# Performance work log

Hardware: AMD Instinct MI355X
Metric: run time of the kernel (lower is better)

The kernel has to match this reference:

```python
import jax, jax.numpy as jnp
import numpy as np

N_NODES = 50000
N_EDGES = 800000
D_FEAT = 128
UNITS = 128


def setup_inputs() -> dict:
    key = jax.random.key(0)
    k1, k2, k3, k4, k5 = jax.random.split(key, 5)
    node_states = jax.random.normal(k1, (N_NODES, D_FEAT), dtype=jnp.float32)
    src = jnp.sort(jax.random.randint(k2, (N_EDGES,), 0, N_NODES))
    dst = jax.random.randint(k3, (N_EDGES,), 0, N_NODES)
    edges = jnp.stack([src, dst], axis=1).astype(jnp.int64)  # [E,2], sorted by source
    kernel = jax.random.normal(k4, (D_FEAT, UNITS), dtype=jnp.float32) * (1.0 / np.sqrt(D_FEAT))
    kernel_attention = jax.random.normal(k5, (2 * UNITS, 1), dtype=jnp.float32) * (1.0 / np.sqrt(2 * UNITS))
    return {"node_states": node_states, "edges": edges, "kernel": kernel, "kernel_attention": kernel_attention}


def reference(node_states, edges, kernel, kernel_attention):
    n_nodes = node_states.shape[0]
    src, dst = edges[:, 0], edges[:, 1]
    # linear transform of node features
    h = node_states @ kernel                                  # [N, U]
    # per-edge concatenated (src, dst) features -> raw attention logit
    e_feat = jnp.concatenate([h[src], h[dst]], axis=-1)       # [E, 2U]
    logits = jax.nn.leaky_relu((e_feat @ kernel_attention)[:, 0], negative_slope=0.2)  # [E]
    scores = jnp.exp(jnp.clip(logits, -2.0, 2.0))             # [E]
    # segment softmax over incoming edges of each source node
    denom = jax.ops.segment_sum(scores, src, num_segments=n_nodes)  # [N]
    alpha = scores / denom[src]                                # [E]
    # weighted aggregation of neighbor features
    out = jax.ops.segment_sum(h[dst] * alpha[:, None], src, num_segments=n_nodes)  # [N, U]
    return out
```

## Files before the change

### kernel.cpp

```cpp
#include <hip/hip_runtime.h>

#define N_NODES 50000
#define N_EDGES 800000
#define D 128
#define LDA 136

typedef __attribute__((ext_vector_type(8))) short bf16x8;
typedef __attribute__((ext_vector_type(4))) float f32x4;

__device__ __forceinline__ unsigned short f2bf(float f) {
    union { float f; unsigned u; } v; v.f = f;
    return (unsigned short)((v.u + 0x7fffu + ((v.u >> 16) & 1u)) >> 16);
}
__device__ __forceinline__ float bflo(unsigned u) {
    union { unsigned u; float f; } c; c.u = u << 16; return c.f;
}
__device__ __forceinline__ float bfhi(unsigned u) {
    union { unsigned u; float f; } c; c.u = u & 0xffff0000u; return c.f;
}

#define NB_SEARCH 196
__global__ void k1_prep(const int* __restrict__ edges, const float* __restrict__ W,
                        const float* __restrict__ ka, int* __restrict__ row_ptr,
                        unsigned short* __restrict__ Wt,
                        float* __restrict__ u, float* __restrict__ v) {
    int b = blockIdx.x, tid = threadIdx.x;
    if (b < NB_SEARCH) {
        int n = b * 256 + tid;
        if (n > N_NODES) return;
        int lo = 0, hi = N_EDGES;
        while (lo < hi) {
            int mid = (lo + hi) >> 1;
            if (edges[2 * mid] < n) lo = mid + 1; else hi = mid;
        }
        row_ptr[n] = lo;
    } else if (b < NB_SEARCH + 8) {
        int bi = b - NB_SEARCH;
        for (int i = tid; i < 16 * D; i += 256) {
            int n = bi * 16 + (i >> 7), k = i & 127;
            Wt[n * D + k] = f2bf(W[k * D + n]);
        }
    } else {
        int k = tid & 127;
        const float* kap = ka + ((tid >> 7) ? D : 0);
        float s = 0.f;
        for (int j = 0; j < D; ++j) s += W[k * D + j] * kap[j];
        if (tid < 128) u[k] = s; else v[k] = s;
    }
}

__global__ __launch_bounds__(256) void kh(const float* __restrict__ X,
                                          const unsigned short* __restrict__ Wt,
                                          const float* __restrict__ u,
                                          const float* __restrict__ v,
                                          unsigned short* __restrict__ h,
                                          float* __restrict__ a_src,
                                          float* __restrict__ a_dst) {
    __shared__ unsigned short As[128 * LDA];
    __shared__ unsigned short Bs[128 * LDA];
    int tid = threadIdx.x;
    int row0 = blockIdx.x * 128;

    for (int i = tid; i < 2048; i += 256) {
        int r = i >> 4, c = i & 15;
        *(uint4*)&Bs[r * LDA + c * 8] = *(const uint4*)&Wt[r * D + c * 8];
    }
    for (int i = tid; i < 2048; i += 256) {
        int r = i >> 4, c = i & 15;
        int gr = row0 + r;
        union { unsigned short us[8]; uint4 q; } pk;
        if (gr < N_NODES) {
            const float* xp = X + (size_t)gr * D + c * 8;
#pragma unroll
            for (int j = 0; j < 8; ++j) pk.us[j] = f2bf(xp[j]);
        } else pk.q = make_uint4(0u, 0u, 0u, 0u);
        *(uint4*)&As[r * LDA + c * 8] = pk.q;
    }
    __syncthreads();

    int wave = tid >> 6, lane = tid & 63;
    int m16 = lane & 15, quad = lane >> 4;
    int wr0 = wave * 32;
    f32x4 acc[2][8];
#pragma unroll
    for (int i = 0; i < 2; ++i)
#pragma unroll
        for (int j = 0; j < 8; ++j) acc[i][j] = (f32x4){0.f, 0.f, 0.f, 0.f};

    for (int k0 = 0; k0 < D; k0 += 32) {
        bf16x8 a0 = *(const bf16x8*)&As[(wr0 + m16) * LDA + k0 + quad * 8];
        bf16x8 a1 = *(const bf16x8*)&As[(wr0 + 16 + m16) * LDA + k0 + quad * 8];
#pragma unroll
        for (int j = 0; j < 8; ++j) {
            bf16x8 bf = *(const bf16x8*)&Bs[(j * 16 + m16) * LDA + k0 + quad * 8];
            acc[0][j] = __builtin_amdgcn_mfma_f32_16x16x32_bf16(a0, bf, acc[0][j], 0, 0, 0);
            acc[1][j] = __builtin_amdgcn_mfma_f32_16x16x32_bf16(a1, bf, acc[1][j], 0, 0, 0);
        }
    }

#pragma unroll
    for (int i = 0; i < 2; ++i)
#pragma unroll
        for (int j = 0; j < 8; ++j)
#pragma unroll
            for (int r = 0; r < 4; ++r) {
                int row = row0 + wr0 + i * 16 + quad * 4 + r;
                if (row < N_NODES)
                    h[(size_t)row * D + j * 16 + m16] = f2bf(acc[i][j][r]);
            }

    int rr = tid >> 1, hf = tid & 1;
    int grow = row0 + rr;
    if (grow < N_NODES) {
        const float* xp = X + (size_t)grow * D + hf * 64;
        float ps = 0.f, pd = 0.f;
        for (int jj = 0; jj < 64; jj += 4) {
            float4 xv = *(const float4*)(xp + jj);
            float4 uv = *(const float4*)(u + hf * 64 + jj);
            float4 vv = *(const float4*)(v + hf * 64 + jj);
            ps += xv.x * uv.x + xv.y * uv.y + xv.z * uv.z + xv.w * uv.w;
            pd += xv.x * vv.x + xv.y * vv.y + xv.z * vv.z + xv.w * vv.w;
        }
        ps += __shfl_xor(ps, 1, 64);
        pd += __shfl_xor(pd, 1, 64);
        if (hf == 0) { a_src[grow] = ps; a_dst[grow] = pd; }
    }
}

__global__ __launch_bounds__(256) void k3(const int* __restrict__ edges,
                                          const int* __restrict__ row_ptr,
                                          const unsigned short* __restrict__ h,
                                          const float* __restrict__ a_src,
                                          const float* __restrict__ a_dst,
                                          float* __restrict__ out) {
    int node = blockIdx.x * 4 + (threadIdx.x >> 6);
    if (node >= N_NODES) return;
    int lane = threadIdx.x & 63;
    int q = lane >> 4;
    int l16 = lane & 15;

    int start = row_ptr[node], end = row_ptr[node + 1];
    float asn = a_src[node];

    float4 accA = make_float4(0.f, 0.f, 0.f, 0.f);
    float4 accB = make_float4(0.f, 0.f, 0.f, 0.f);
    float dn = 0.f;

    for (int base = start; base < end; base += 64) {
        int cnt = min(64, end - base);
        int d = 0; float s = 0.f;
        if (lane < cnt) {
            d = edges[2 * (base + lane) + 1];
            float lg = asn + a_dst[d];
            lg = (lg >= 0.f) ? lg : 0.2f * lg;
            lg = fminf(fmaxf(lg, -2.f), 2.f);
            s = __expf(lg);
        }
        for (int j = 0; j < cnt; j += 8) {
            float s0 = __shfl(s, j + q, 64);
            int   d0 = __shfl(d, j + q, 64);
            float s1 = __shfl(s, j + q + 4, 64);
            int   d1 = __shfl(d, j + q + 4, 64);
            uint4 p0 = *(const uint4*)(h + ((size_t)d0 << 7) + (l16 << 3));
            uint4 p1 = *(const uint4*)(h + ((size_t)d1 << 7) + (l16 << 3));
            accA.x += s0 * bflo(p0.x); accA.y += s0 * bfhi(p0.x);
            accA.z += s0 * bflo(p0.y); accA.w += s0 * bfhi(p0.y);
            accB.x += s0 * bflo(p0.z); accB.y += s0 * bfhi(p0.z);
            accB.z += s0 * bflo(p0.w); accB.w += s0 * bfhi(p0.w);
            accA.x += s1 * bflo(p1.x); accA.y += s1 * bfhi(p1.x);
            accA.z += s1 * bflo(p1.y); accA.w += s1 * bfhi(p1.y);
            accB.x += s1 * bflo(p1.z); accB.y += s1 * bfhi(p1.z);
            accB.z += s1 * bflo(p1.w); accB.w += s1 * bfhi(p1.w);
            dn += s0 + s1;
        }
    }

    float vals[9] = {accA.x, accA.y, accA.z, accA.w,
                     accB.x, accB.y, accB.z, accB.w, dn};
#pragma unroll
    for (int m = 32; m >= 16; m >>= 1)
#pragma unroll
        for (int i = 0; i < 9; ++i) vals[i] += __shfl_xor(vals[i], m, 64);

    if (q == 0) {
        float inv = (end > start) ? 1.f / vals[8] : 0.f;
        float4 o0 = make_float4(vals[0] * inv, vals[1] * inv, vals[2] * inv, vals[3] * inv);
        float4 o1 = make_float4(vals[4] * inv, vals[5] * inv, vals[6] * inv, vals[7] * inv);
        float* op = out + (size_t)node * D + l16 * 8;
        *(float4*)op = o0;
        *(float4*)(op + 4) = o1;
    }
}

extern "C" void kernel_launch(void* const* d_in, const int* in_sizes, int n_in,
                              void* d_out, int out_size, void* d_ws, size_t ws_size,
                              hipStream_t stream) {
    const float* X     = (const float*)d_in[0];
    const int*   edges = (const int*)d_in[1];
    const float* W     = (const float*)d_in[2];
    const float* ka    = (const float*)d_in[3];

    char* ws = (char*)d_ws;
    unsigned short* h  = (unsigned short*)ws;
    float* a_src   = (float*)(ws + (size_t)N_NODES * D * 2);
    float* a_dst   = a_src + N_NODES;
    int*   row_ptr = (int*)(a_dst + N_NODES);
    unsigned short* Wt = (unsigned short*)(row_ptr + N_NODES + 4);
    float* u = (float*)(Wt + D * D);
    float* v = u + D;
    float* out = (float*)d_out;

    k1_prep<<<NB_SEARCH + 9, 256, 0, stream>>>(edges, W, ka, row_ptr, Wt, u, v);
    kh<<<(N_NODES + 127) / 128, 256, 0, stream>>>(X, Wt, u, v, h, a_src, a_dst);
    k3<<<(N_NODES + 3) / 4, 256, 0, stream>>>(edges, row_ptr, h, a_src, a_dst, out);
}
```

Baseline: 134.3 us.

## Fuse prep into GEMM kernel, derive attention logits from accumulators, widen gather

Merges the row-pointer search, weight transpose and projection into the GEMM kernel, so one launch handles both and every block converts W into shared memory itself. The per-node attention terms now come from the MFMA accumulators dotted with the attention vector, replacing a second read of X against precomputed u/v. The aggregation loop now issues four row gathers per iteration instead of two to get more loads in flight. The cost is redundant W conversion in every GEMM block, strided 2-byte LDS writes during that conversion, and attention logits computed from the bf16-rounded GEMM result instead of full-precision X.

```diff
diff --git a/kernel.cpp b/kernel.cpp
--- a/kernel.cpp
+++ b/kernel.cpp
@@ -5,6 +5,9 @@
 #define D 128
 #define LDA 136
 
+#define SEARCH_BLOCKS 196
+#define GEMM_BLOCKS   391
+
 typedef __attribute__((ext_vector_type(8))) short bf16x8;
 typedef __attribute__((ext_vector_type(4))) float f32x4;
 
@@ -19,13 +22,20 @@
     union { unsigned u; float f; } c; c.u = u & 0xffff0000u; return c.f;
 }
 
-#define NB_SEARCH 196
-__global__ void k1_prep(const int* __restrict__ edges, const float* __restrict__ W,
-                        const float* __restrict__ ka, int* __restrict__ row_ptr,
-                        unsigned short* __restrict__ Wt,
-                        float* __restrict__ u, float* __restrict__ v) {
+__global__ __launch_bounds__(256) void kh_fused(const float* __restrict__ X,
+                                                const int* __restrict__ edges,
+                                                const float* __restrict__ W,
+                                                const float* __restrict__ ka,
+                                                unsigned short* __restrict__ h,
+                                                float* __restrict__ a_src,
+                                                float* __restrict__ a_dst,
+                                                int* __restrict__ row_ptr) {
+    __shared__ unsigned short As[128 * LDA];
+    __shared__ unsigned short Bs[128 * LDA];
+    __shared__ float kas[2 * D];
     int b = blockIdx.x, tid = threadIdx.x;
-    if (b < NB_SEARCH) {
+
+    if (b < SEARCH_BLOCKS) {
         int n = b * 256 + tid;
         if (n > N_NODES) return;
         int lo = 0, hi = N_EDGES;
@@ -34,36 +44,18 @@
             if (edges[2 * mid] < n) lo = mid + 1; else hi = mid;
         }
         row_ptr[n] = lo;
-    } else if (b < NB_SEARCH + 8) {
-        int bi = b - NB_SEARCH;
-        for (int i = tid; i < 16 * D; i += 256) {
-            int n = bi * 16 + (i >> 7), k = i & 127;
-            Wt[n * D + k] = f2bf(W[k * D + n]);
-        }
-    } else {
-        int k = tid & 127;
-        const float* kap = ka + ((tid >> 7) ? D : 0);
-        float s = 0.f;
-        for (int j = 0; j < D; ++j) s += W[k * D + j] * kap[j];
-        if (tid < 128) u[k] = s; else v[k] = s;
-    }
-}
-
-__global__ __launch_bounds__(256) void kh(const float* __restrict__ X,
-                                          const unsigned short* __restrict__ Wt,
-                                          const float* __restrict__ u,
-                                          const float* __restrict__ v,
-                                          unsigned short* __restrict__ h,
-                                          float* __restrict__ a_src,
-                                          float* __restrict__ a_dst) {
-    __shared__ unsigned short As[128 * LDA];
-    __shared__ unsigned short Bs[128 * LDA];
-    int tid = threadIdx.x;
-    int row0 = blockIdx.x * 128;
-
-    for (int i = tid; i < 2048; i += 256) {
-        int r = i >> 4, c = i & 15;
-        *(uint4*)&Bs[r * LDA + c * 8] = *(const uint4*)&Wt[r * D + c * 8];
+        return;
+    }
+
+    int row0 = (b - SEARCH_BLOCKS) * 128;
+    kas[tid] = ka[tid];
+    for (int i = tid; i < 128 * 32; i += 256) {
+        int k = i >> 5, n4 = (i & 31) * 4;
+        float4 w = *(const float4*)(W + k * D + n4);
+        Bs[(n4 + 0) * LDA + k] = f2bf(w.x);
+        Bs[(n4 + 1) * LDA + k] = f2bf(w.y);
+        Bs[(n4 + 2) * LDA + k] = f2bf(w.z);
+        Bs[(n4 + 3) * LDA + k] = f2bf(w.w);
     }
     for (int i = tid; i < 2048; i += 256) {
         int r = i >> 4, c = i & 15;
@@ -109,22 +101,24 @@
                     h[(size_t)row * D + j * 16 + m16] = f2bf(acc[i][j][r]);
             }
 
-    int rr = tid >> 1, hf = tid & 1;
-    int grow = row0 + rr;
-    if (grow < N_NODES) {
-        const float* xp = X + (size_t)grow * D + hf * 64;
-        float ps = 0.f, pd = 0.f;
-        for (int jj = 0; jj < 64; jj += 4) {
-            float4 xv = *(const float4*)(xp + jj);
-            float4 uv = *(const float4*)(u + hf * 64 + jj);
-            float4 vv = *(const float4*)(v + hf * 64 + jj);
-            ps += xv.x * uv.x + xv.y * uv.y + xv.z * uv.z + xv.w * uv.w;
-            pd += xv.x * vv.x + xv.y * vv.y + xv.z * vv.z + xv.w * vv.w;
-        }
-        ps += __shfl_xor(ps, 1, 64);
-        pd += __shfl_xor(pd, 1, 64);
-        if (hf == 0) { a_src[grow] = ps; a_dst[grow] = pd; }
-    }
+#pragma unroll
+    for (int i = 0; i < 2; ++i)
+#pragma unroll
+        for (int r = 0; r < 4; ++r) {
+            float ps = 0.f, pd = 0.f;
+#pragma unroll
+            for (int j = 0; j < 8; ++j) {
+                float val = acc[i][j][r];
+                ps += val * kas[j * 16 + m16];
+                pd += val * kas[D + j * 16 + m16];
+            }
+            for (int off = 8; off > 0; off >>= 1) {
+                ps += __shfl_down(ps, off, 16);
+                pd += __shfl_down(pd, off, 16);
+            }
+            int row = row0 + wr0 + i * 16 + quad * 4 + r;
+            if (m16 == 0 && row < N_NODES) { a_src[row] = ps; a_dst[row] = pd; }
+        }
 }
 
 __global__ __launch_bounds__(256) void k3(const int* __restrict__ edges,
@@ -156,22 +150,26 @@
             lg = fminf(fmaxf(lg, -2.f), 2.f);
             s = __expf(lg);
         }
-        for (int j = 0; j < cnt; j += 8) {
-            float s0 = __shfl(s, j + q, 64);
-            int   d0 = __shfl(d, j + q, 64);
-            float s1 = __shfl(s, j + q + 4, 64);
-            int   d1 = __shfl(d, j + q + 4, 64);
-            uint4 p0 = *(const uint4*)(h + ((size_t)d0 << 7) + (l16 << 3));
-            uint4 p1 = *(const uint4*)(h + ((size_t)d1 << 7) + (l16 << 3));
-            accA.x += s0 * bflo(p0.x); accA.y += s0 * bfhi(p0.x);
-            accA.z += s0 * bflo(p0.y); accA.w += s0 * bfhi(p0.y);
-            accB.x += s0 * bflo(p0.z); accB.y += s0 * bfhi(p0.z);
-            accB.z += s0 * bflo(p0.w); accB.w += s0 * bfhi(p0.w);
-            accA.x += s1 * bflo(p1.x); accA.y += s1 * bfhi(p1.x);
-            accA.z += s1 * bflo(p1.y); accA.w += s1 * bfhi(p1.y);
-            accB.x += s1 * bflo(p1.z); accB.y += s1 * bfhi(p1.z);
-            accB.z += s1 * bflo(p1.w); accB.w += s1 * bfhi(p1.w);
-            dn += s0 + s1;
+        for (int j = 0; j < cnt; j += 16) {
+            float sj[4]; int dj[4];
+#pragma unroll
+            for (int t = 0; t < 4; ++t) {
+                sj[t] = __shfl(s, j + q + 4 * t, 64);
+                dj[t] = __shfl(d, j + q + 4 * t, 64);
+            }
+            uint4 p[4];
+#pragma unroll
+            for (int t = 0; t < 4; ++t)
+                p[t] = *(const uint4*)(h + ((size_t)dj[t] << 7) + (l16 << 3));
+#pragma unroll
+            for (int t = 0; t < 4; ++t) {
+                float sv = sj[t];
+                accA.x += sv * bflo(p[t].x); accA.y += sv * bfhi(p[t].x);
+                accA.z += sv * bflo(p[t].y); accA.w += sv * bfhi(p[t].y);
+                accB.x += sv * bflo(p[t].z); accB.y += sv * bfhi(p[t].z);
+                accB.z += sv * bflo(p[t].w); accB.w += sv * bfhi(p[t].w);
+                dn += sv;
+            }
         }
     }
 
@@ -205,12 +203,9 @@
     float* a_src   = (float*)(ws + (size_t)N_NODES * D * 2);
     float* a_dst   = a_src + N_NODES;
     int*   row_ptr = (int*)(a_dst + N_NODES);
-    unsigned short* Wt = (unsigned short*)(row_ptr + N_NODES + 4);
-    float* u = (float*)(Wt + D * D);
-    float* v = u + D;
     float* out = (float*)d_out;
 
-    k1_prep<<<NB_SEARCH + 9, 256, 0, stream>>>(edges, W, ka, row_ptr, Wt, u, v);
-    kh<<<(N_NODES + 127) / 128, 256, 0, stream>>>(X, Wt, u, v, h, a_src, a_dst);
+    kh_fused<<<SEARCH_BLOCKS + GEMM_BLOCKS, 256, 0, stream>>>(
+        X, edges, W, ka, h, a_src, a_dst, row_ptr);
     k3<<<(N_NODES + 3) / 4, 256, 0, stream>>>(edges, row_ptr, h, a_src, a_dst, out);
 }
```

Result: faster. 127.5 us (-5.0%).
